# Performance work log

Hardware: AMD Instinct MI355X
Metric: run time of the kernel (lower is better)

## Reference

```python
import jax, jax.numpy as jnp
import numpy as np

NA = 100000
NB = 100000
E = 500000
D = 256
EPS = 1e-5


def setup_inputs() -> dict:
    key = jax.random.key(0)
    ks = jax.random.split(key, 10)
    scale = 1.0 / np.sqrt(D)
    return {
        "feat_a": jax.random.normal(ks[0], (NA, D), jnp.float32),
        "feat_b": jax.random.normal(ks[1], (NB, D), jnp.float32),
        "src_ab": jax.random.randint(ks[2], (E,), 0, NA, jnp.int32),
        "dst_ab": jax.random.randint(ks[3], (E,), 0, NB, jnp.int32),
        "src_ba": jax.random.randint(ks[4], (E,), 0, NB, jnp.int32),
        "dst_ba": jax.random.randint(ks[5], (E,), 0, NA, jnp.int32),
        "WT_ab": jax.random.normal(ks[6], (D, D), jnp.float32) * scale,
        "WT_ba": jax.random.normal(ks[7], (D, D), jnp.float32) * scale,
        "WA_ab": jax.random.normal(ks[8], (1, D), jnp.float32) * scale,
        "WA_ba": jax.random.normal(ks[9], (1, D), jnp.float32) * scale,
        "gamma": jnp.ones((D,), jnp.float32),
        "beta": jnp.zeros((D,), jnp.float32),
    }


def _etype_agg(h_src, h_dst, src, dst, WT, WA, n_dst):
    # per-etype linear on src nodes: t_h = W_T h_src
    t_h = h_src @ WT.T                              # [Ns, D]
    x = t_h[src] * h_dst[dst]                       # u_mul_v -> [E, D]
    s = jnp.exp(x @ WA.T)                           # exp(W_A x) -> [E, 1]
    att_sum = jax.ops.segment_sum(s, dst, num_segments=n_dst)  # copy_e+sum
    att = s / att_sum[dst]                          # e_div_v (dst of an edge always has >=1 edge)
    # u_mul_e + sum: weighted scatter of raw src features
    return jax.ops.segment_sum(h_src[src] * att, dst, num_segments=n_dst)


def _finalize(h, gamma, beta):
    h = jax.nn.relu(h)
    mu = jnp.mean(h, axis=-1, keepdims=True)
    var = jnp.mean(jnp.square(h - mu), axis=-1, keepdims=True)
    return (h - mu) / jnp.sqrt(var + EPS) * gamma + beta  # dropout is identity (eval)


def reference(feat_a, feat_b, src_ab, dst_ab, src_ba, dst_ba,
              WT_ab, WT_ba, WA_ab, WA_ba, gamma, beta):
    h_b = _etype_agg(feat_a, feat_b, src_ab, dst_ab, WT_ab, WA_ab, NB)
    h_a = _etype_agg(feat_b, feat_a, src_ba, dst_ba, WT_ba, WA_ba, NA)
    out_a = _finalize(h_a, gamma, beta)
    out_b = _finalize(h_b, gamma, beta)
    return jnp.stack([out_a, out_b])  # [2, N, D]
```

## Files before the change

kernel.cpp:

```cpp
#include <hip/hip_runtime.h>
#include <hip/hip_bf16.h>

#define D 256

typedef __attribute__((ext_vector_type(8))) short short8;
typedef __attribute__((ext_vector_type(4))) float f32x4;
typedef __attribute__((ext_vector_type(4))) unsigned short u16x4;

__device__ __forceinline__ unsigned short f2bf(float f) {
  unsigned int u = __builtin_bit_cast(unsigned int, f);
  u = (u + 0x7FFFu + ((u >> 16) & 1u)) >> 16;
  return (unsigned short)u;
}
__device__ __forceinline__ float bf2f(unsigned short h) {
  unsigned int u = ((unsigned int)h) << 16;
  return __builtin_bit_cast(float, u);
}

__device__ __forceinline__ float wred(float x) {
  float t;
#define DPP_STEP(ctrl, rmask)                                                  \
  t = __builtin_bit_cast(float, __builtin_amdgcn_update_dpp(                   \
          0, __builtin_bit_cast(int, x), (ctrl), (rmask), 0xf, true));         \
  x += t;
  DPP_STEP(0x111, 0xf)
  DPP_STEP(0x112, 0xf)
  DPP_STEP(0x114, 0xf)
  DPP_STEP(0x118, 0xf)
  DPP_STEP(0x142, 0xa)
  DPP_STEP(0x143, 0xc)
#undef DPP_STEP
  return __builtin_bit_cast(float, __builtin_amdgcn_readlane(__builtin_bit_cast(int, x), 63));
}

__global__ void zero_f32(float* __restrict__ p, int n) {
  int i = blockIdx.x * 256 + threadIdx.x;
  if (i < n) p[i] = 0.f;
}
__global__ void zero2_k(int* __restrict__ a, int na, int* __restrict__ b, int nb) {
  int i = blockIdx.x * 256 + threadIdx.x;
  if (i < na) a[i] = 0;
  else if (i - na < nb) b[i - na] = 0;
}

__global__ void classify_k(const float* __restrict__ q0, const float* __restrict__ q1,
                           const float* __restrict__ q2, const float* __restrict__ q3,
                           int* __restrict__ flags) {
  __shared__ int cnt1[4], cnt0[4];
  int t = threadIdx.x;
  if (t < 4) { cnt1[t] = 0; cnt0[t] = 0; }
  __syncthreads();
  const float* qs[4] = {q0, q1, q2, q3};
#pragma unroll
  for (int v = 0; v < 4; ++v) {
    float x = qs[v][t];
    if (x == 1.0f) atomicAdd(&cnt1[v], 1);
    if (x == 0.0f) atomicAdd(&cnt0[v], 1);
  }
  __syncthreads();
  if (t == 0) {
    int gi = -1, bi = -1;
    for (int v = 0; v < 4; ++v) if (cnt1[v] == 256 && gi < 0) gi = v;
    for (int v = 0; v < 4; ++v) if (cnt0[v] == 256 && v != gi && bi < 0) bi = v;
    if (gi < 0) gi = 2;
    if (bi < 0) bi = (gi == 3) ? 2 : 3;
    int wa[2], w = 0;
    for (int v = 0; v < 4; ++v) if (v != gi && v != bi) { if (w < 2) wa[w] = v; ++w; }
    flags[0] = wa[0]; flags[1] = wa[1]; flags[2] = gi; flags[3] = bi;
  }
}

__global__ void prep_w2(const float* __restrict__ WT_ab, const float* __restrict__ WT_ba,
                        const float* __restrict__ q0, const float* __restrict__ q1,
                        const float* __restrict__ q2, const float* __restrict__ q3,
                        const int* __restrict__ flags,
                        unsigned short* __restrict__ w2ab, unsigned short* __restrict__ w2ba) {
  const float* qs[4] = {q0, q1, q2, q3};
  const float* WAab = qs[flags[0]];
  const float* WAba = qs[flags[1]];
  int i = blockIdx.x * 256 + threadIdx.x;
  int n = i >> 8;
  w2ab[i] = f2bf(WAab[n] * WT_ab[i]);
  w2ba[i] = f2bf(WAba[n] * WT_ba[i]);
}

__global__ void prep_w2z(const float* __restrict__ WT_ab, const float* __restrict__ WT_ba,
                         const float* __restrict__ q0, const float* __restrict__ q1,
                         const float* __restrict__ q2, const float* __restrict__ q3,
                         const int* __restrict__ flags,
                         unsigned short* __restrict__ zab, unsigned short* __restrict__ zba) {
  const float* qs[4] = {q0, q1, q2, q3};
  const float* WAab = qs[flags[0]];
  const float* WAba = qs[flags[1]];
  int i = blockIdx.x * 256 + threadIdx.x;
  int c = i >> 8, d = i & 255;
  zab[i] = f2bf(WAab[d] * WT_ab[d * 256 + c]);
  zba[i] = f2bf(WAba[d] * WT_ba[d * 256 + c]);
}

__device__ __forceinline__ void gemm_body(const float* feat, const unsigned short* w2,
                                          unsigned short* g, unsigned short* featbf,
                                          int nchunks, int do_featbf, int cb,
                                          unsigned char* bl0, unsigned char* bl1) {
  int lane = threadIdx.x & 63;
  int wv = threadIdx.x >> 6;
  int c0 = cb * 8 + wv;
  bool active = c0 < nchunks;
  int c = active ? c0 : (nchunks - 1);
  int r16 = lane & 15;
  int kg = lane >> 4;
  int row0 = c * 32;

  short8 a[2][8];
#pragma unroll
  for (int sub = 0; sub < 2; ++sub) {
    int row = row0 + sub * 16 + r16;
    const float* rp = feat + (size_t)row * D + kg * 8;
#pragma unroll
    for (int kk = 0; kk < 8; ++kk) {
      f32x4 x0 = *(const f32x4*)(rp + kk * 32);
      f32x4 x1 = *(const f32x4*)(rp + kk * 32 + 4);
      short8 t;
      t[0] = (short)f2bf(x0[0]); t[1] = (short)f2bf(x0[1]);
      t[2] = (short)f2bf(x0[2]); t[3] = (short)f2bf(x0[3]);
      t[4] = (short)f2bf(x1[0]); t[5] = (short)f2bf(x1[1]);
      t[6] = (short)f2bf(x1[2]); t[7] = (short)f2bf(x1[3]);
      a[sub][kk] = t;
      if (do_featbf && active)
        *(short8*)(featbf + (size_t)row * D + kk * 32 + kg * 8) = t;
    }
  }

  int t = threadIdx.x;
  int brow = t >> 5, bc = t & 31;
  int slin = brow * 512 + bc * 16;
  int sswz = slin ^ ((brow & 7) << 4);

  *(short8*)(bl0 + sswz) = *(const short8*)(w2 + (size_t)brow * D + bc * 8);
  __syncthreads();

  unsigned char* bl[2] = {bl0, bl1};
  int cur = 0;
#pragma unroll 1
  for (int nt = 0; nt < 16; ++nt) {
    short8 tnext;
    bool has = nt + 1 < 16;
    if (has)
      tnext = *(const short8*)(w2 + (size_t)((nt + 1) * 16 + brow) * D + bc * 8);

    f32x4 acc0 = {0.f, 0.f, 0.f, 0.f};
    f32x4 acc1 = {0.f, 0.f, 0.f, 0.f};
    const unsigned char* blc = bl[cur];
#pragma unroll
    for (int kk = 0; kk < 8; ++kk) {
      int lin = r16 * 512 + kk * 64 + kg * 16;
      int swz = lin ^ ((r16 & 7) << 4);
      short8 b = *(const short8*)(blc + swz);
      acc0 = __builtin_amdgcn_mfma_f32_16x16x32_bf16(a[0][kk], b, acc0, 0, 0, 0);
      acc1 = __builtin_amdgcn_mfma_f32_16x16x32_bf16(a[1][kk], b, acc1, 0, 0, 0);
    }
    if (active) {
      int colv = nt * 16 + r16;
#pragma unroll
      for (int j = 0; j < 4; ++j) {
        int r = row0 + kg * 4 + j;
        g[(size_t)r * D + colv] = f2bf(acc0[j]);
        g[(size_t)(r + 16) * D + colv] = f2bf(acc1[j]);
      }
    }
    if (has) *(short8*)(bl[cur ^ 1] + sswz) = tnext;
    __syncthreads();
    cur ^= 1;
  }
}

__global__ __launch_bounds__(512) void gemm_g(const float* __restrict__ feat,
                                              const unsigned short* __restrict__ w2,
                                              unsigned short* __restrict__ g,
                                              unsigned short* __restrict__ featbf,
                                              int nchunks, int do_featbf) {
  __shared__ __align__(16) unsigned char bl[2][8192];
  gemm_body(feat, w2, g, featbf, nchunks, do_featbf, blockIdx.x, bl[0], bl[1]);
}

__global__ __launch_bounds__(512) void gemm2_g(const float* __restrict__ feat_a,
                                               const float* __restrict__ feat_b,
                                               const unsigned short* __restrict__ w2z_ab,
                                               const unsigned short* __restrict__ w2z_ba,
                                               unsigned short* __restrict__ z_a,
                                               unsigned short* __restrict__ z_b,
                                               unsigned short* __restrict__ fbf_a,
                                               unsigned short* __restrict__ fbf_b,
                                               int chA, int chB) {
  __shared__ __align__(16) unsigned char bl[2][8192];
  int nblkA = (chA + 7) / 8;
  bool isA = (int)blockIdx.x < nblkA;
  const float* feat = isA ? feat_a : feat_b;
  const unsigned short* w2 = isA ? w2z_ba : w2z_ab;
  unsigned short* z = isA ? z_a : z_b;
  unsigned short* fbf = isA ? fbf_a : fbf_b;
  int nchunks = isA ? chA : chB;
  int cb = isA ? blockIdx.x : blockIdx.x - nblkA;
  gemm_body(feat, w2, z, fbf, nchunks, 1, cb, bl[0], bl[1]);
}

__global__ void hist2_k(const int* __restrict__ dab, int* __restrict__ degb,
                        const int* __restrict__ dba, int* __restrict__ dega, int E) {
  int i = blockIdx.x * blockDim.x + threadIdx.x;
  if (i < E) atomicAdd(&degb[dab[i]], 1);
  else if (i - E < E) atomicAdd(&dega[dba[i - E]], 1);
}

__global__ void scanA2_k(const int* __restrict__ degb, int* __restrict__ rpb,
                         int* __restrict__ bsb, int nB,
                         const int* __restrict__ dega, int* __restrict__ rpa,
                         int* __restrict__ bsa, int nA, int nbB) {
  __shared__ int sh[1024];
  bool isB = (int)blockIdx.x < nbB;
  const int* deg = isB ? degb : dega;
  int* rp = isB ? rpb : rpa;
  int* bsum = isB ? bsb : bsa;
  int n = isB ? nB : nA;
  int blk = isB ? blockIdx.x : blockIdx.x - nbB;
  int i = blk * 1024 + threadIdx.x;
  int v = (i < n) ? deg[i] : 0;
  sh[threadIdx.x] = v;
  __syncthreads();
  for (int off = 1; off < 1024; off <<= 1) {
    int tv = (threadIdx.x >= (unsigned)off) ? sh[threadIdx.x - off] : 0;
    __syncthreads();
    sh[threadIdx.x] += tv;
    __syncthreads();
  }
  if (i < n) rp[i] = sh[threadIdx.x] - v;
  if (threadIdx.x == 1023) bsum[blk] = sh[1023];
}

__global__ void scanB_k(int* __restrict__ bsB, int* __restrict__ bsA, int nbB, int nbA) {
  __shared__ int sh[128];
  int* b = (blockIdx.x == 0) ? bsB : bsA;
  int nb = (blockIdx.x == 0) ? nbB : nbA;
  int t = threadIdx.x;
  int v = (t < nb) ? b[t] : 0;
  sh[t] = v;
  __syncthreads();
  for (int off = 1; off < 128; off <<= 1) {
    int u = (t >= off) ? sh[t - off] : 0;
    __syncthreads();
    sh[t] += u;
    __syncthreads();
  }
  if (t < nb) b[t] = sh[t] - v;
}

__global__ void scanC2_k(int* __restrict__ rpb, int* __restrict__ curb,
                         const int* __restrict__ bsb, int nB,
                         int* __restrict__ rpa, int* __restrict__ cura,
                         const int* __restrict__ bsa, int nA, int nbB, int E) {
  bool isB = (int)blockIdx.x < nbB;
  int* rp = isB ? rpb : rpa;
  int* cursor = isB ? curb : cura;
  const int* bsum = isB ? bsb : bsa;
  int n = isB ? nB : nA;
  int blk = isB ? blockIdx.x : blockIdx.x - nbB;
  int i = blk * 1024 + threadIdx.x;
  if (i < n) {
    int v = rp[i] + bsum[i >> 10];
    rp[i] = v;
    cursor[i] = v;
  }
  if (i == 0) rp[n] = E;
}

__global__ void scatter2_k(const int* __restrict__ sab, const int* __restrict__ dab,
                           int* __restrict__ curb, int* __restrict__ colab,
                           const int* __restrict__ sba, const int* __restrict__ dba,
                           int* __restrict__ cura, int* __restrict__ colba, int E) {
  int i = blockIdx.x * blockDim.x + threadIdx.x;
  if (i < E) {
    int slot = atomicAdd(&curb[dab[i]], 1);
    colab[slot] = sab[i];
  } else if (i - E < E) {
    int j = i - E;
    int slot = atomicAdd(&cura[dba[j]], 1);
    colba[slot] = sba[j];
  }
}

__global__ __launch_bounds__(256) void aggz_k(const unsigned short* __restrict__ fbf_a,
                                              const unsigned short* __restrict__ fbf_b,
                                              const unsigned short* __restrict__ z_a,
                                              const unsigned short* __restrict__ z_b,
                                              const int* __restrict__ rp_a,
                                              const int* __restrict__ rp_b,
                                              const int* __restrict__ col_ab,
                                              const int* __restrict__ col_ba,
                                              const float* __restrict__ q0,
                                              const float* __restrict__ q1,
                                              const float* __restrict__ q2,
                                              const float* __restrict__ q3,
                                              const int* __restrict__ flags,
                                              float* __restrict__ out_a,
                                              float* __restrict__ out_b,
                                              int NA, int NB) {
  const float* qs[4] = {q0, q1, q2, q3};
  const float* gamma = qs[flags[2]];
  const float* beta  = qs[flags[3]];
  int gB = (NB + 3) / 4;
  bool isB = (int)blockIdx.x < gB;
  const unsigned short* fsrc = isB ? fbf_a : fbf_b;
  const unsigned short* z    = isB ? z_b  : z_a;
  const int* rp  = isB ? rp_b : rp_a;
  const int* col = isB ? col_ab : col_ba;
  float* out = isB ? out_b : out_a;
  int n_dst = isB ? NB : NA;
  int vb = isB ? blockIdx.x : blockIdx.x - gB;

  int lane = threadIdx.x & 63;
  int v = vb * 4 + (threadIdx.x >> 6);
  if (v >= n_dst) return;
  u16x4 zq = *(const u16x4*)(z + (size_t)v * D + lane * 4);
  f32x4 zv;
  zv[0] = bf2f(zq[0]); zv[1] = bf2f(zq[1]); zv[2] = bf2f(zq[2]); zv[3] = bf2f(zq[3]);
  int beg = rp[v], end = rp[v + 1];

  float ssum = 0.f;
  f32x4 acc = {0.f, 0.f, 0.f, 0.f};
  int i = beg;
  for (; i + 3 < end; i += 4) {
    int sc0 = col[i], sc1 = col[i + 1], sc2 = col[i + 2], sc3 = col[i + 3];
    u16x4 q0v = *(const u16x4*)(fsrc + (size_t)sc0 * D + lane * 4);
    u16x4 q1v = *(const u16x4*)(fsrc + (size_t)sc1 * D + lane * 4);
    u16x4 q2v = *(const u16x4*)(fsrc + (size_t)sc2 * D + lane * 4);
    u16x4 q3v = *(const u16x4*)(fsrc + (size_t)sc3 * D + lane * 4);
    f32x4 f0, f1, f2, f3;
#pragma unroll
    for (int j = 0; j < 4; ++j) {
      f0[j] = bf2f(q0v[j]); f1[j] = bf2f(q1v[j]);
      f2[j] = bf2f(q2v[j]); f3[j] = bf2f(q3v[j]);
    }
    float d0 = f0[0] * zv[0] + f0[1] * zv[1] + f0[2] * zv[2] + f0[3] * zv[3];
    float d1 = f1[0] * zv[0] + f1[1] * zv[1] + f1[2] * zv[2] + f1[3] * zv[3];
    float d2 = f2[0] * zv[0] + f2[1] * zv[1] + f2[2] * zv[2] + f2[3] * zv[3];
    float d3 = f3[0] * zv[0] + f3[1] * zv[1] + f3[2] * zv[2] + f3[3] * zv[3];
    d0 = wred(d0); d1 = wred(d1); d2 = wred(d2); d3 = wred(d3);
    float s0 = __expf(d0), s1 = __expf(d1), s2 = __expf(d2), s3 = __expf(d3);
    ssum += (s0 + s1) + (s2 + s3);
#pragma unroll
    for (int j = 0; j < 4; ++j)
      acc[j] += f0[j] * s0 + f1[j] * s1 + f2[j] * s2 + f3[j] * s3;
  }
  for (; i < end; ++i) {
    int sc = col[i];
    u16x4 fq = *(const u16x4*)(fsrc + (size_t)sc * D + lane * 4);
    f32x4 f;
    f[0] = bf2f(fq[0]); f[1] = bf2f(fq[1]); f[2] = bf2f(fq[2]); f[3] = bf2f(fq[3]);
    float d = f[0] * zv[0] + f[1] * zv[1] + f[2] * zv[2] + f[3] * zv[3];
    d = wred(d);
    float s = __expf(d);
    ssum += s;
    acc[0] += f[0] * s; acc[1] += f[1] * s;
    acc[2] += f[2] * s; acc[3] += f[3] * s;
  }
  float inv = (end > beg) ? (1.f / ssum) : 0.f;
  acc[0] *= inv; acc[1] *= inv; acc[2] *= inv; acc[3] *= inv;

  acc[0] = fmaxf(acc[0], 0.f); acc[1] = fmaxf(acc[1], 0.f);
  acc[2] = fmaxf(acc[2], 0.f); acc[3] = fmaxf(acc[3], 0.f);

  float sm = wred(acc[0] + acc[1] + acc[2] + acc[3]);
  float mu = sm * (1.f / 256.f);
  f32x4 dl;
  dl[0] = acc[0] - mu; dl[1] = acc[1] - mu; dl[2] = acc[2] - mu; dl[3] = acc[3] - mu;
  float sq = wred(dl[0] * dl[0] + dl[1] * dl[1] + dl[2] * dl[2] + dl[3] * dl[3]);
  float rs = rsqrtf(sq * (1.f / 256.f) + 1e-5f);

  f32x4 gm = *(const f32x4*)(gamma + lane * 4);
  f32x4 bt = *(const f32x4*)(beta + lane * 4);
  f32x4 o;
  o[0] = dl[0] * rs * gm[0] + bt[0];
  o[1] = dl[1] * rs * gm[1] + bt[1];
  o[2] = dl[2] * rs * gm[2] + bt[2];
  o[3] = dl[3] * rs * gm[3] + bt[3];
  *(f32x4*)(out + (size_t)v * D + lane * 4) = o;
}

__global__ __launch_bounds__(256) void agg_ln_bf(const unsigned short* __restrict__ fsrc,
                                                 const float* __restrict__ feat_dst,
                                                 const unsigned short* __restrict__ g,
                                                 const int* __restrict__ rp,
                                                 const int* __restrict__ colsrc,
                                                 const float* __restrict__ q0,
                                                 const float* __restrict__ q1,
                                                 const float* __restrict__ q2,
                                                 const float* __restrict__ q3,
                                                 const int* __restrict__ flags,
                                                 float* __restrict__ out, int n_dst) {
  const float* qs[4] = {q0, q1, q2, q3};
  const float* gamma = qs[flags[2]];
  const float* beta  = qs[flags[3]];
  int lane = threadIdx.x & 63;
  int v = blockIdx.x * 4 + (threadIdx.x >> 6);
  if (v >= n_dst) return;
  f32x4 hv = *(const f32x4*)(feat_dst + (size_t)v * D + lane * 4);
  int beg = rp[v], end = rp[v + 1];

  float ssum = 0.f;
  f32x4 acc = {0.f, 0.f, 0.f, 0.f};
  if (beg < end) {
    int sc = colsrc[beg];
    u16x4 gq = *(const u16x4*)(g + (size_t)sc * D + lane * 4);
    u16x4 fq = *(const u16x4*)(fsrc + (size_t)sc * D + lane * 4);
    for (int i = beg; i < end; ++i) {
      int ip = (i + 1 < end) ? (i + 1) : i;
      int scn = colsrc[ip];
      u16x4 gqn = *(const u16x4*)(g + (size_t)scn * D + lane * 4);
      u16x4 fqn = *(const u16x4*)(fsrc + (size_t)scn * D + lane * 4);
      float d = bf2f(gq[0]) * hv[0] + bf2f(gq[1]) * hv[1] +
                bf2f(gq[2]) * hv[2] + bf2f(gq[3]) * hv[3];
#pragma unroll
      for (int off = 32; off > 0; off >>= 1) d += __shfl_xor(d, off, 64);
      float s = __expf(d);
      ssum += s;
      acc[0] += bf2f(fq[0]) * s; acc[1] += bf2f(fq[1]) * s;
      acc[2] += bf2f(fq[2]) * s; acc[3] += bf2f(fq[3]) * s;
      gq = gqn; fq = fqn;
    }
  }
  float inv = (end > beg) ? (1.f / ssum) : 0.f;
  acc[0] *= inv; acc[1] *= inv; acc[2] *= inv; acc[3] *= inv;

  acc[0] = fmaxf(acc[0], 0.f); acc[1] = fmaxf(acc[1], 0.f);
  acc[2] = fmaxf(acc[2], 0.f); acc[3] = fmaxf(acc[3], 0.f);

  float sm = acc[0] + acc[1] + acc[2] + acc[3];
#pragma unroll
  for (int off = 32; off > 0; off >>= 1) sm += __shfl_xor(sm, off, 64);
  float mu = sm * (1.f / 256.f);
  f32x4 dl;
  dl[0] = acc[0] - mu; dl[1] = acc[1] - mu; dl[2] = acc[2] - mu; dl[3] = acc[3] - mu;
  float sq = dl[0] * dl[0] + dl[1] * dl[1] + dl[2] * dl[2] + dl[3] * dl[3];
#pragma unroll
  for (int off = 32; off > 0; off >>= 1) sq += __shfl_xor(sq, off, 64);
  float rs = rsqrtf(sq * (1.f / 256.f) + 1e-5f);

  f32x4 gm = *(const f32x4*)(gamma + lane * 4);
  f32x4 bt = *(const f32x4*)(beta + lane * 4);
  f32x4 o;
  o[0] = dl[0] * rs * gm[0] + bt[0];
  o[1] = dl[1] * rs * gm[1] + bt[1];
  o[2] = dl[2] * rs * gm[2] + bt[2];
  o[3] = dl[3] * rs * gm[3] + bt[3];
  *(f32x4*)(out + (size_t)v * D + lane * 4) = o;
}

__global__ __launch_bounds__(256) void agg_ln(const float* __restrict__ feat_src,
                                              const float* __restrict__ feat_dst,
                                              const unsigned short* __restrict__ g,
                                              const int* __restrict__ rp,
                                              const int* __restrict__ colsrc,
                                              const float* __restrict__ q0,
                                              const float* __restrict__ q1,
                                              const float* __restrict__ q2,
                                              const float* __restrict__ q3,
                                              const int* __restrict__ flags,
                                              float* __restrict__ out, int n_dst) {
  const float* qs[4] = {q0, q1, q2, q3};
  const float* gamma = qs[flags[2]];
  const float* beta  = qs[flags[3]];
  int lane = threadIdx.x & 63;
  int v = blockIdx.x * 4 + (threadIdx.x >> 6);
  if (v >= n_dst) return;
  f32x4 hv = *(const f32x4*)(feat_dst + (size_t)v * D + lane * 4);
  int beg = rp[v], end = rp[v + 1];

  float ssum = 0.f;
  f32x4 acc = {0.f, 0.f, 0.f, 0.f};
  for (int i = beg; i < end; ++i) {
    int sc = colsrc[i];
    u16x4 gq = *(const u16x4*)(g + (size_t)sc * D + lane * 4);
    float d = bf2f(gq[0]) * hv[0] + bf2f(gq[1]) * hv[1] +
              bf2f(gq[2]) * hv[2] + bf2f(gq[3]) * hv[3];
#pragma unroll
    for (int off = 32; off > 0; off >>= 1) d += __shfl_xor(d, off, 64);
    float s = __expf(d);
    ssum += s;
    f32x4 f = *(const f32x4*)(feat_src + (size_t)sc * D + lane * 4);
    acc[0] += f[0] * s; acc[1] += f[1] * s;
    acc[2] += f[2] * s; acc[3] += f[3] * s;
  }
  float inv = (end > beg) ? (1.f / ssum) : 0.f;
  acc[0] *= inv; acc[1] *= inv; acc[2] *= inv; acc[3] *= inv;

  acc[0] = fmaxf(acc[0], 0.f); acc[1] = fmaxf(acc[1], 0.f);
  acc[2] = fmaxf(acc[2], 0.f); acc[3] = fmaxf(acc[3], 0.f);

  float sm = acc[0] + acc[1] + acc[2] + acc[3];
#pragma unroll
  for (int off = 32; off > 0; off >>= 1) sm += __shfl_xor(sm, off, 64);
  float mu = sm * (1.f / 256.f);
  f32x4 dl;
  dl[0] = acc[0] - mu; dl[1] = acc[1] - mu; dl[2] = acc[2] - mu; dl[3] = acc[3] - mu;
  float sq = dl[0] * dl[0] + dl[1] * dl[1] + dl[2] * dl[2] + dl[3] * dl[3];
#pragma unroll
  for (int off = 32; off > 0; off >>= 1) sq += __shfl_xor(sq, off, 64);
  float rs = rsqrtf(sq * (1.f / 256.f) + 1e-5f);

  f32x4 gm = *(const f32x4*)(gamma + lane * 4);
  f32x4 bt = *(const f32x4*)(beta + lane * 4);
  f32x4 o;
  o[0] = dl[0] * rs * gm[0] + bt[0];
  o[1] = dl[1] * rs * gm[1] + bt[1];
  o[2] = dl[2] * rs * gm[2] + bt[2];
  o[3] = dl[3] * rs * gm[3] + bt[3];
  *(f32x4*)(out + (size_t)v * D + lane * 4) = o;
}

extern "C" void kernel_launch(void* const* d_in, const int* in_sizes, int n_in,
                              void* d_out, int out_size, void* d_ws, size_t ws_size,
                              hipStream_t stream) {
  const float* feat_a = (const float*)d_in[0];
  const float* feat_b = (const float*)d_in[1];
  const int* src_ab = (const int*)d_in[2];
  const int* dst_ab = (const int*)d_in[3];
  const int* src_ba = (const int*)d_in[4];
  const int* dst_ba = (const int*)d_in[5];
  const float* WT_ab = (const float*)d_in[6];
  const float* WT_ba = (const float*)d_in[7];
  const float* q0 = (const float*)d_in[8];
  const float* q1 = (const float*)d_in[9];
  const float* q2 = (const float*)d_in[10];
  const float* q3 = (const float*)d_in[11];

  int NA = in_sizes[0] / D;
  int NB = in_sizes[1] / D;
  int E = in_sizes[2];

  float* out = (float*)d_out;
  float* out_a = out;
  float* out_b = out + (size_t)NA * D;

  char* w = (char*)d_ws;
  size_t off = 0;
  auto alloc = [&](size_t bytes) -> void* {
    void* p = (void*)(w + off);
    off += (bytes + 255) & ~(size_t)255;
    return p;
  };
  size_t nmax = (size_t)(NA > NB ? NA : NB);
  unsigned short* gws = (unsigned short*)alloc(nmax * D * 2);
  unsigned short* w2ab = (unsigned short*)alloc(65536 * 2);
  unsigned short* w2ba = (unsigned short*)alloc(65536 * 2);
  unsigned short* w2z_ab = (unsigned short*)alloc(65536 * 2);
  unsigned short* w2z_ba = (unsigned short*)alloc(65536 * 2);
  int* dc_b = (int*)alloc((size_t)NB * 4);
  int* dc_a = (int*)alloc((size_t)NA * 4);
  int* rp_b = (int*)alloc((size_t)(NB + 1) * 4);
  int* rp_a = (int*)alloc((size_t)(NA + 1) * 4);
  int* col_ab = (int*)alloc((size_t)E * 4);
  int* col_ba = (int*)alloc((size_t)E * 4);
  int* bs_b = (int*)alloc(512);
  int* bs_a = (int*)alloc(512);
  int* flags = (int*)alloc(256);
  size_t need_base = off;
  unsigned short* featbf = (unsigned short*)alloc(nmax * D * 2);
  size_t need_full = off;
  unsigned short* z_a = (unsigned short*)alloc(nmax * D * 2);
  unsigned short* featbf2 = (unsigned short*)alloc(nmax * D * 2);
  size_t need_z = off;

  bool bad = (n_in != 12);
  bad = bad || (in_sizes[0] != in_sizes[1]);
  bad = bad || (in_sizes[2] != in_sizes[3]) || (in_sizes[3] != in_sizes[4]) ||
        (in_sizes[4] != in_sizes[5]);
  bad = bad || (in_sizes[6] != 65536) || (in_sizes[7] != 65536);
  bad = bad || (in_sizes[8] != 256) || (in_sizes[9] != 256) ||
        (in_sizes[10] != 256) || (in_sizes[11] != 256);
  bad = bad || (out_size != (NA + NB) * D);
  bad = bad || (ws_size < need_base);
  if (bad) {
    zero_f32<<<(out_size + 255) / 256, 256, 0, stream>>>(out, out_size);
    return;
  }
  int zplan = (ws_size >= need_z)    ? 1 : 0;
  int fast  = (ws_size >= need_full) ? 1 : 0;

  classify_k<<<1, 256, 0, stream>>>(q0, q1, q2, q3, flags);
  zero2_k<<<(NA + NB + 255) / 256, 256, 0, stream>>>(dc_b, NB, dc_a, NA);
  if (zplan)
    prep_w2z<<<256, 256, 0, stream>>>(WT_ab, WT_ba, q0, q1, q2, q3, flags,
                                      w2z_ab, w2z_ba);
  else
    prep_w2<<<256, 256, 0, stream>>>(WT_ab, WT_ba, q0, q1, q2, q3, flags,
                                     w2ab, w2ba);

  hist2_k<<<(2 * E + 255) / 256, 256, 0, stream>>>(dst_ab, dc_b, dst_ba, dc_a, E);

  int nbB = (NB + 1023) / 1024, nbA = (NA + 1023) / 1024;
  scanA2_k<<<nbB + nbA, 1024, 0, stream>>>(dc_b, rp_b, bs_b, NB,
                                           dc_a, rp_a, bs_a, NA, nbB);
  scanB_k<<<2, 128, 0, stream>>>(bs_b, bs_a, nbB, nbA);
  scanC2_k<<<nbB + nbA, 1024, 0, stream>>>(rp_b, dc_b, bs_b, NB,
                                           rp_a, dc_a, bs_a, NA, nbB, E);
  scatter2_k<<<(2 * E + 255) / 256, 256, 0, stream>>>(src_ab, dst_ab, dc_b, col_ab,
                                                      src_ba, dst_ba, dc_a, col_ba, E);

  int chA = (NA + 31) / 32, chB = (NB + 31) / 32;

  if (zplan) {
    int nblk = (chA + 7) / 8 + (chB + 7) / 8;
    gemm2_g<<<nblk, 512, 0, stream>>>(feat_a, feat_b, w2z_ab, w2z_ba,
                                      z_a, gws , featbf ,
                                      featbf2 , chA, chB);
    int gtot = (NB + 3) / 4 + (NA + 3) / 4;
    aggz_k<<<gtot, 256, 0, stream>>>(featbf, featbf2, z_a, gws ,
                                     rp_a, rp_b, col_ab, col_ba,
                                     q0, q1, q2, q3, flags, out_a, out_b, NA, NB);
  } else if (fast) {
    gemm_g<<<(chA + 7) / 8, 512, 0, stream>>>(feat_a, w2ab, gws, featbf, chA, 1);
    agg_ln_bf<<<(NB + 3) / 4, 256, 0, stream>>>(featbf, feat_b, gws, rp_b, col_ab,
                                                q0, q1, q2, q3, flags, out_b, NB);
    gemm_g<<<(chB + 7) / 8, 512, 0, stream>>>(feat_b, w2ba, gws, featbf, chB, 1);
    agg_ln_bf<<<(NA + 3) / 4, 256, 0, stream>>>(featbf, feat_a, gws, rp_a, col_ba,
                                                q0, q1, q2, q3, flags, out_a, NA);
  } else {
    gemm_g<<<(chA + 7) / 8, 512, 0, stream>>>(feat_a, w2ab, gws, gws, chA, 0);
    agg_ln<<<(NB + 3) / 4, 256, 0, stream>>>(feat_a, feat_b, gws, rp_b, col_ab,
                                             q0, q1, q2, q3, flags, out_b, NB);
    gemm_g<<<(chB + 7) / 8, 512, 0, stream>>>(feat_b, w2ba, gws, gws, chB, 0);
    agg_ln<<<(NA + 3) / 4, 256, 0, stream>>>(feat_b, feat_a, gws, rp_a, col_ba,
                                             q0, q1, q2, q3, flags, out_a, NA);
  }
}
```

Before: 430.3 us.

## Gather fp32 source features directly and broadcast edge indices via readlane

The GEMM stage no longer writes bf16 copies of the node features. The aggregation kernel instead gathers the original fp32 rows, which doubles the bytes per gathered row but removes the bf16 conversion writes and the extra buffer. For nodes with degree up to 64, each wave loads the column indices once with a coalesced read and broadcasts them with readlane, instead of issuing scalar index loads per edge. The workspace layout is also reordered so the z plan needs less memory. This trades more gather traffic for fewer write passes and less index-load latency.

After: 409.6 us. -4.8%, faster.

```diff
diff --git a/kernel.cpp b/kernel.cpp
--- a/kernel.cpp
+++ b/kernel.cpp
@@ -189,8 +189,6 @@
                                                const unsigned short* __restrict__ w2z_ba,
                                                unsigned short* __restrict__ z_a,
                                                unsigned short* __restrict__ z_b,
-                                               unsigned short* __restrict__ fbf_a,
-                                               unsigned short* __restrict__ fbf_b,
                                                int chA, int chB) {
   __shared__ __align__(16) unsigned char bl[2][8192];
   int nblkA = (chA + 7) / 8;
@@ -198,10 +196,9 @@
   const float* feat = isA ? feat_a : feat_b;
   const unsigned short* w2 = isA ? w2z_ba : w2z_ab;
   unsigned short* z = isA ? z_a : z_b;
-  unsigned short* fbf = isA ? fbf_a : fbf_b;
   int nchunks = isA ? chA : chB;
   int cb = isA ? blockIdx.x : blockIdx.x - nblkA;
-  gemm_body(feat, w2, z, fbf, nchunks, 1, cb, bl[0], bl[1]);
+  gemm_body(feat, w2, z, z, nchunks, 0, cb, bl[0], bl[1]);
 }
 
 __global__ void hist2_k(const int* __restrict__ dab, int* __restrict__ degb,
@@ -287,8 +284,8 @@
   }
 }
 
-__global__ __launch_bounds__(256) void aggz_k(const unsigned short* __restrict__ fbf_a,
-                                              const unsigned short* __restrict__ fbf_b,
+__global__ __launch_bounds__(256) void aggz_k(const float* __restrict__ feat_a,
+                                              const float* __restrict__ feat_b,
                                               const unsigned short* __restrict__ z_a,
                                               const unsigned short* __restrict__ z_b,
                                               const int* __restrict__ rp_a,
@@ -308,8 +305,8 @@
   const float* beta  = qs[flags[3]];
   int gB = (NB + 3) / 4;
   bool isB = (int)blockIdx.x < gB;
-  const unsigned short* fsrc = isB ? fbf_a : fbf_b;
-  const unsigned short* z    = isB ? z_b  : z_a;
+  const float* fsrc = isB ? feat_a : feat_b;
+  const unsigned short* z = isB ? z_b : z_a;
   const int* rp  = isB ? rp_b : rp_a;
   const int* col = isB ? col_ab : col_ba;
   float* out = isB ? out_b : out_a;
@@ -323,46 +320,57 @@
   f32x4 zv;
   zv[0] = bf2f(zq[0]); zv[1] = bf2f(zq[1]); zv[2] = bf2f(zq[2]); zv[3] = bf2f(zq[3]);
   int beg = rp[v], end = rp[v + 1];
+  int deg = end - beg;
+  const float* fbase = fsrc + lane * 4;
 
   float ssum = 0.f;
   f32x4 acc = {0.f, 0.f, 0.f, 0.f};
-  int i = beg;
-  for (; i + 3 < end; i += 4) {
-    int sc0 = col[i], sc1 = col[i + 1], sc2 = col[i + 2], sc3 = col[i + 3];
-    u16x4 q0v = *(const u16x4*)(fsrc + (size_t)sc0 * D + lane * 4);
-    u16x4 q1v = *(const u16x4*)(fsrc + (size_t)sc1 * D + lane * 4);
-    u16x4 q2v = *(const u16x4*)(fsrc + (size_t)sc2 * D + lane * 4);
-    u16x4 q3v = *(const u16x4*)(fsrc + (size_t)sc3 * D + lane * 4);
-    f32x4 f0, f1, f2, f3;
-#pragma unroll
-    for (int j = 0; j < 4; ++j) {
-      f0[j] = bf2f(q0v[j]); f1[j] = bf2f(q1v[j]);
-      f2[j] = bf2f(q2v[j]); f3[j] = bf2f(q3v[j]);
+  if (deg > 0 && deg <= 64) {
+    int colv = col[beg + (lane < deg ? lane : deg - 1)];
+    int i = 0;
+    for (; i + 3 < deg; i += 4) {
+      int sc0 = __builtin_amdgcn_readlane(colv, i);
+      int sc1 = __builtin_amdgcn_readlane(colv, i + 1);
+      int sc2 = __builtin_amdgcn_readlane(colv, i + 2);
+      int sc3 = __builtin_amdgcn_readlane(colv, i + 3);
+      f32x4 f0 = *(const f32x4*)(fbase + (size_t)sc0 * D);
+      f32x4 f1 = *(const f32x4*)(fbase + (size_t)sc1 * D);
+      f32x4 f2 = *(const f32x4*)(fbase + (size_t)sc2 * D);
+      f32x4 f3 = *(const f32x4*)(fbase + (size_t)sc3 * D);
+      float d0 = f0[0] * zv[0] + f0[1] * zv[1] + f0[2] * zv[2] + f0[3] * zv[3];
+      float d1 = f1[0] * zv[0] + f1[1] * zv[1] + f1[2] * zv[2] + f1[3] * zv[3];
+      float d2 = f2[0] * zv[0] + f2[1] * zv[1] + f2[2] * zv[2] + f2[3] * zv[3];
+      float d3 = f3[0] * zv[0] + f3[1] * zv[1] + f3[2] * zv[2] + f3[3] * zv[3];
+      d0 = wred(d0); d1 = wred(d1); d2 = wred(d2); d3 = wred(d3);
+      float s0 = __expf(d0), s1 = __expf(d1), s2 = __expf(d2), s3 = __expf(d3);
+      ssum += (s0 + s1) + (s2 + s3);
+#pragma unroll
+      for (int j = 0; j < 4; ++j)
+        acc[j] += f0[j] * s0 + f1[j] * s1 + f2[j] * s2 + f3[j] * s3;
     }
-    float d0 = f0[0] * zv[0] + f0[1] * zv[1] + f0[2] * zv[2] + f0[3] * zv[3];
-    float d1 = f1[0] * zv[0] + f1[1] * zv[1] + f1[2] * zv[2] + f1[3] * zv[3];
-    float d2 = f2[0] * zv[0] + f2[1] * zv[1] + f2[2] * zv[2] + f2[3] * zv[3];
-    float d3 = f3[0] * zv[0] + f3[1] * zv[1] + f3[2] * zv[2] + f3[3] * zv[3];
-    d0 = wred(d0); d1 = wred(d1); d2 = wred(d2); d3 = wred(d3);
-    float s0 = __expf(d0), s1 = __expf(d1), s2 = __expf(d2), s3 = __expf(d3);
-    ssum += (s0 + s1) + (s2 + s3);
-#pragma unroll
-    for (int j = 0; j < 4; ++j)
-      acc[j] += f0[j] * s0 + f1[j] * s1 + f2[j] * s2 + f3[j] * s3;
-  }
-  for (; i < end; ++i) {
-    int sc = col[i];
-    u16x4 fq = *(const u16x4*)(fsrc + (size_t)sc * D + lane * 4);
-    f32x4 f;
-    f[0] = bf2f(fq[0]); f[1] = bf2f(fq[1]); f[2] = bf2f(fq[2]); f[3] = bf2f(fq[3]);
-    float d = f[0] * zv[0] + f[1] * zv[1] + f[2] * zv[2] + f[3] * zv[3];
-    d = wred(d);
-    float s = __expf(d);
-    ssum += s;
-    acc[0] += f[0] * s; acc[1] += f[1] * s;
-    acc[2] += f[2] * s; acc[3] += f[3] * s;
-  }
-  float inv = (end > beg) ? (1.f / ssum) : 0.f;
+    for (; i < deg; ++i) {
+      int sc = __builtin_amdgcn_readlane(colv, i);
+      f32x4 f = *(const f32x4*)(fbase + (size_t)sc * D);
+      float d = f[0] * zv[0] + f[1] * zv[1] + f[2] * zv[2] + f[3] * zv[3];
+      d = wred(d);
+      float s = __expf(d);
+      ssum += s;
+      acc[0] += f[0] * s; acc[1] += f[1] * s;
+      acc[2] += f[2] * s; acc[3] += f[3] * s;
+    }
+  } else if (deg > 64) {
+    for (int i = beg; i < end; ++i) {
+      int sc = col[i];
+      f32x4 f = *(const f32x4*)(fbase + (size_t)sc * D);
+      float d = f[0] * zv[0] + f[1] * zv[1] + f[2] * zv[2] + f[3] * zv[3];
+      d = wred(d);
+      float s = __expf(d);
+      ssum += s;
+      acc[0] += f[0] * s; acc[1] += f[1] * s;
+      acc[2] += f[2] * s; acc[3] += f[3] * s;
+    }
+  }
+  float inv = (deg > 0) ? (1.f / ssum) : 0.f;
   acc[0] *= inv; acc[1] *= inv; acc[2] *= inv; acc[3] *= inv;
 
   acc[0] = fmaxf(acc[0], 0.f); acc[1] = fmaxf(acc[1], 0.f);
@@ -563,11 +571,10 @@
   int* bs_a = (int*)alloc(512);
   int* flags = (int*)alloc(256);
   size_t need_base = off;
+  unsigned short* z_a = (unsigned short*)alloc(nmax * D * 2);
+  size_t need_z = off;
   unsigned short* featbf = (unsigned short*)alloc(nmax * D * 2);
   size_t need_full = off;
-  unsigned short* z_a = (unsigned short*)alloc(nmax * D * 2);
-  unsigned short* featbf2 = (unsigned short*)alloc(nmax * D * 2);
-  size_t need_z = off;
 
   bool bad = (n_in != 12);
   bad = bad || (in_sizes[0] != in_sizes[1]);
@@ -610,10 +617,9 @@
   if (zplan) {
     int nblk = (chA + 7) / 8 + (chB + 7) / 8;
     gemm2_g<<<nblk, 512, 0, stream>>>(feat_a, feat_b, w2z_ab, w2z_ba,
-                                      z_a, gws , featbf ,
-                                      featbf2 , chA, chB);
+                                      z_a, gws , chA, chB);
     int gtot = (NB + 3) / 4 + (NA + 3) / 4;
-    aggz_k<<<gtot, 256, 0, stream>>>(featbf, featbf2, z_a, gws ,
+    aggz_k<<<gtot, 256, 0, stream>>>(feat_a, feat_b, z_a, gws ,
                                      rp_a, rp_b, col_ab, col_ba,
                                      q0, q1, q2, q3, flags, out_a, out_b, NA, NB);
   } else if (fast) {
```
